# Performance work log

Hardware: AMD Instinct MI355X
Metric: run time of the kernel (lower is better)

The kernel has to match this reference:

```python
import jax, jax.numpy as jnp
import numpy as np

B, D, C = 32768, 1024, 40  # batch, proj_dim, num_classes('culture')


def setup_inputs() -> dict:
    key = jax.random.key(0)
    k1, k2, k3, k4, k5 = jax.random.split(key, 5)
    scale = 1.0 / np.sqrt(D)
    return {
        "src": jax.random.normal(k1, (B, D), dtype=jnp.float32),
        "attn_mask": jnp.ones((B,), dtype=jnp.float32),  # unpacked but unused by BiChain
        # padded weights: row i uses only first D+i columns; the rest hit zero buffer slots
        "W": jax.random.normal(k2, (C, D + C), dtype=jnp.float32) * scale,
        "b": jax.random.normal(k3, (C,), dtype=jnp.float32) * scale,
        "W_rev": jax.random.normal(k4, (C, D + C), dtype=jnp.float32) * scale,
        "b_rev": jax.random.normal(k5, (C,), dtype=jnp.float32) * scale,
    }


def _chain(src, W, b):
    """Sequential classifier chain: score_i = sigmoid(<[src, s_0..s_{i-1}], w_i> + b_i)."""
    Bsz, Df = src.shape
    Cn = W.shape[0]
    # growing feature buffer, pre-padded with zeros for future scores
    buf0 = jnp.zeros((Bsz, Df + Cn), dtype=src.dtype).at[:, :Df].set(src)

    def step(buf, inp):
        w_i, b_i, i = inp
        score = jax.nn.sigmoid(buf @ w_i + b_i)            # [B]
        buf = jax.lax.dynamic_update_slice(buf, score[:, None], (0, Df + i))
        return buf, score

    _, scores = jax.lax.scan(step, buf0, (W, b, jnp.arange(Cn)))
    return scores.T  # [B, C]


def reference(src, attn_mask, W, b, W_rev, b_rev):
    out_fwd = _chain(src, W, b)
    out_rev = _chain(src, W_rev, b_rev)
    return (out_fwd + out_rev[:, ::-1]) * 0.5
```

## Files before the change

kernel.cpp:

```cpp
#include <hip/hip_runtime.h>
#include <hip/hip_bf16.h>
#include <math.h>

using short8  = __attribute__((ext_vector_type(8))) short;
using float4v = __attribute__((ext_vector_type(4))) float;

#define D_DIM 1024
#define NCLS  40
#define WSTR  1064
#define TM    64
#define NCHUNK 16

typedef const __attribute__((address_space(1))) void g_void;
typedef __attribute__((address_space(3))) void lds_void;

__device__ __forceinline__ short f2bf(float f) {
    __hip_bfloat16 h = __float2bfloat16(f);
    union { __hip_bfloat16 h; short s; } u; u.h = h;
    return u.s;
}

__global__ void convert_w_kernel(const float* __restrict__ W, const float* __restrict__ Wr,
                                 short* __restrict__ Wfrag) {
    int idx  = blockIdx.x * 256 + threadIdx.x;
    int lane = idx & 63;
    int rest = idx >> 6;
    int t    = rest % 5;
    int rest2 = rest / 5;
    int ks   = rest2 & 1;
    int ch   = rest2 >> 1;
    int cls  = t * 16 + (lane & 15);
    int k0   = ch * 64 + ks * 32 + (lane >> 4) * 8;
    const float* srow = (cls < NCLS) ? (W + (size_t)cls * WSTR)
                                     : (Wr + (size_t)(cls - NCLS) * WSTR);
    short8 v;
#pragma unroll
    for (int e = 0; e < 8; ++e) v[e] = f2bf(srow[k0 + e]);
    *(short8*)(Wfrag + (size_t)idx * 8) = v;
}

__global__ __launch_bounds__(256, 2) void bichain_main(
    const float* __restrict__ src, const short* __restrict__ Wfrag,
    const float* __restrict__ Wf, const float* __restrict__ Wr,
    const float* __restrict__ bf_, const float* __restrict__ br_,
    float* __restrict__ out)
{
    __shared__ __align__(16) char smem[32768];

    const int tid  = threadIdx.x;
    const int lane = tid & 63;
    const int wave = tid >> 6;
    const int row0 = blockIdx.x * TM;
    const int lrow = lane & 15;
    const int g4   = lane >> 4;

    float4v acc[5];
#pragma unroll
    for (int t = 0; t < 5; ++t)
#pragma unroll
        for (int r = 0; r < 4; ++r) acc[t][r] = 0.f;

    auto stage = [&](int ch, int buf) {
        char* dst0 = smem + buf * 16384 + wave * 4096;
#pragma unroll
        for (int j = 0; j < 4; ++j) {
            int r   = wave * 16 + j * 4 + g4;
            int j16 = lrow ^ (r & 7);
            const float* gp = src + (size_t)(row0 + r) * D_DIM + ch * 64 + j16 * 4;
            __builtin_amdgcn_global_load_lds((g_void*)gp, (lds_void*)(dst0 + j * 1024),
                                             16, 0, 0);
        }
    };

    stage(0, 0);
    __syncthreads();

#pragma unroll 2
    for (int ch = 0; ch < NCHUNK; ++ch) {
        const int buf = ch & 1;
        short8 wfr[2][5];
#pragma unroll
        for (int ks = 0; ks < 2; ++ks)
#pragma unroll
            for (int t = 0; t < 5; ++t)
                wfr[ks][t] = *(const short8*)(Wfrag +
                                (((size_t)(ch * 2 + ks) * 5 + t) << 9) + (lane << 3));
        if (ch < NCHUNK - 1) stage(ch + 1, buf ^ 1);

        const char* Ab = smem + buf * 16384 + (wave * 16 + lrow) * 256;
#pragma unroll
        for (int ks = 0; ks < 2; ++ks) {
            float4v f0 = *(const float4v*)(Ab + (((ks * 8 + g4 * 2 + 0) ^ (lrow & 7)) << 4));
            float4v f1 = *(const float4v*)(Ab + (((ks * 8 + g4 * 2 + 1) ^ (lrow & 7)) << 4));
            short8 af;
#pragma unroll
            for (int e = 0; e < 4; ++e) { af[e] = f2bf(f0[e]); af[e + 4] = f2bf(f1[e]); }
#pragma unroll
            for (int t = 0; t < 5; ++t)
                acc[t] = __builtin_amdgcn_mfma_f32_16x16x32_bf16(af, wfr[ks][t], acc[t], 0, 0, 0);
        }
        __syncthreads();
    }

    float* Lg = (float*)smem;
#pragma unroll
    for (int t = 0; t < 5; ++t)
#pragma unroll
        for (int r = 0; r < 4; ++r) {
            int row = wave * 16 + g4 * 4 + r;
            int cls = t * 16 + lrow;
            Lg[row * 81 + cls] = acc[t][r];
        }
    __syncthreads();

    if (tid < 128) {
        const int row = tid >> 1;
        const int dir = tid & 1;
        const float* Wt = dir ? Wr : Wf;
        const float* bi = dir ? br_ : bf_;
        float s[NCLS];
#pragma unroll
        for (int i = 0; i < NCLS; ++i) {
            float z = Lg[row * 81 + dir * NCLS + i] + bi[i];
#pragma unroll
            for (int j = 0; j < i; ++j)
                z += s[j] * Wt[i * WSTR + D_DIM + j];
            s[i] = 1.f / (1.f + __expf(-z));
            Lg[row * 81 + dir * NCLS + i] = s[i];
        }
    }
    __syncthreads();

    float* outp = out + (size_t)row0 * NCLS;
    for (int idx = tid; idx < TM * NCLS; idx += 256) {
        int row = idx / NCLS;
        int c   = idx - row * NCLS;
        outp[idx] = 0.5f * (Lg[row * 81 + c] + Lg[row * 81 + NCLS + (NCLS - 1 - c)]);
    }
}

extern "C" void kernel_launch(void* const* d_in, const int* in_sizes, int n_in,
                              void* d_out, int out_size, void* d_ws, size_t ws_size,
                              hipStream_t stream) {
    const float* src = (const float*)d_in[0];
    const float* W   = (const float*)d_in[2];
    const float* b   = (const float*)d_in[3];
    const float* Wr  = (const float*)d_in[4];
    const float* br  = (const float*)d_in[5];
    float* out = (float*)d_out;
    short* Wfrag = (short*)d_ws;

    convert_w_kernel<<<40, 256, 0, stream>>>(W, Wr, Wfrag);
    bichain_main<<<512, 256, 0, stream>>>(src, Wfrag, W, Wr, b, br, out);
}
```

Before: 45.31 us.

## Replace LDS DMA staging with register-prefetched, wave-private bf16 LDS ring

The block-wide double-buffered global_load_lds staging of fp32 activations is replaced by register prefetch three chunks ahead. Each wave converts its rows to bf16 and writes them into its own private three-slot LDS ring, with the weight fragments double-buffered in registers. Because each wave only reads its own LDS slice, the per-chunk __syncthreads is removed, and the loop is fully unrolled to keep more global loads in flight. The cost is much higher register pressure from the prefetch arrays, which could lower occupancy below the launch-bounds target or cause spills.

```diff
diff --git a/kernel.cpp b/kernel.cpp
--- a/kernel.cpp
+++ b/kernel.cpp
@@ -2,17 +2,15 @@
 #include <hip/hip_bf16.h>
 #include <math.h>
 
-using short8  = __attribute__((ext_vector_type(8))) short;
-using float4v = __attribute__((ext_vector_type(4))) float;
+using short8   = __attribute__((ext_vector_type(8))) short;
+using ushort4v = __attribute__((ext_vector_type(4))) unsigned short;
+using float4v  = __attribute__((ext_vector_type(4))) float;
 
 #define D_DIM 1024
 #define NCLS  40
 #define WSTR  1064
 #define TM    64
-#define NCHUNK 16
-
-typedef const __attribute__((address_space(1))) void g_void;
-typedef __attribute__((address_space(3))) void lds_void;
+#define NCH   16
 
 __device__ __forceinline__ short f2bf(float f) {
     __hip_bfloat16 h = __float2bfloat16(f);
@@ -45,70 +43,99 @@
     const float* __restrict__ bf_, const float* __restrict__ br_,
     float* __restrict__ out)
 {
-    __shared__ __align__(16) char smem[32768];
+    __shared__ __align__(16) char smem[24576];
 
     const int tid  = threadIdx.x;
     const int lane = tid & 63;
     const int wave = tid >> 6;
     const int row0 = blockIdx.x * TM;
-    const int lrow = lane & 15;
-    const int g4   = lane >> 4;
+    const int i16  = lane & 15;
+    const int i4   = lane >> 4;
 
+    char* ldsW = smem + wave * 6144;
+    const float* aGlob = src + (size_t)(row0 + wave * 16 + i4) * D_DIM + i16 * 4;
+
+    float4v ap[3][4];
+    short8  wp[2][10];
     float4v acc[5];
 #pragma unroll
     for (int t = 0; t < 5; ++t)
 #pragma unroll
         for (int r = 0; r < 4; ++r) acc[t][r] = 0.f;
 
-    auto stage = [&](int ch, int buf) {
-        char* dst0 = smem + buf * 16384 + wave * 4096;
-#pragma unroll
-        for (int j = 0; j < 4; ++j) {
-            int r   = wave * 16 + j * 4 + g4;
-            int j16 = lrow ^ (r & 7);
-            const float* gp = src + (size_t)(row0 + r) * D_DIM + ch * 64 + j16 * 4;
-            __builtin_amdgcn_global_load_lds((g_void*)gp, (lds_void*)(dst0 + j * 1024),
-                                             16, 0, 0);
-        }
-    };
+#define LOADA(ch) do { if ((ch) < NCH) {                                   \
+    const float* _p = aGlob + (ch) * 64;                                   \
+    ap[(ch)%3][0] = *(const float4v*)(_p);                                 \
+    ap[(ch)%3][1] = *(const float4v*)(_p + 4 * D_DIM);                     \
+    ap[(ch)%3][2] = *(const float4v*)(_p + 8 * D_DIM);                     \
+    ap[(ch)%3][3] = *(const float4v*)(_p + 12 * D_DIM); } } while (0)
 
-    stage(0, 0);
+#define LOADW(ch) do { if ((ch) < NCH) {                                   \
+    const short* _w = Wfrag + (size_t)(ch) * 5120 + (lane << 3);           \
+    wp[(ch)%2][0] = *(const short8*)(_w + 0 * 512);                        \
+    wp[(ch)%2][1] = *(const short8*)(_w + 1 * 512);                        \
+    wp[(ch)%2][2] = *(const short8*)(_w + 2 * 512);                        \
+    wp[(ch)%2][3] = *(const short8*)(_w + 3 * 512);                        \
+    wp[(ch)%2][4] = *(const short8*)(_w + 4 * 512);                        \
+    wp[(ch)%2][5] = *(const short8*)(_w + 5 * 512);                        \
+    wp[(ch)%2][6] = *(const short8*)(_w + 6 * 512);                        \
+    wp[(ch)%2][7] = *(const short8*)(_w + 7 * 512);                        \
+    wp[(ch)%2][8] = *(const short8*)(_w + 8 * 512);                        \
+    wp[(ch)%2][9] = *(const short8*)(_w + 9 * 512); } } while (0)
+
+#define DSW1(ch, j) {                                                      \
+    int _r = (j) * 4 + i4;                                                 \
+    ushort4v _v;                                                           \
+    _v[0] = (unsigned short)f2bf(ap[(ch)%3][j][0]);                        \
+    _v[1] = (unsigned short)f2bf(ap[(ch)%3][j][1]);                        \
+    _v[2] = (unsigned short)f2bf(ap[(ch)%3][j][2]);                        \
+    _v[3] = (unsigned short)f2bf(ap[(ch)%3][j][3]);                        \
+    *(ushort4v*)(_b + _r * 128 + ((i16 ^ ((_r & 7) << 1)) << 3)) = _v; }
+#define DSW(ch) do { if ((ch) < NCH) {                                     \
+    char* _b = ldsW + ((ch)%3) * 2048;                                     \
+    DSW1(ch, 0) DSW1(ch, 1) DSW1(ch, 2) DSW1(ch, 3) } } while (0)
+
+#define MFMA_(ch) do {                                                     \
+    const char* _fb = ldsW + ((ch)%3) * 2048 + i16 * 128;                  \
+    const int _sw = (i16 & 7) << 1;                                        \
+    short8 _a0 = *(const short8*)(_fb + (((i4 * 2)     ^ _sw) << 3));      \
+    acc[0] = __builtin_amdgcn_mfma_f32_16x16x32_bf16(_a0, wp[(ch)%2][0], acc[0], 0, 0, 0); \
+    acc[1] = __builtin_amdgcn_mfma_f32_16x16x32_bf16(_a0, wp[(ch)%2][1], acc[1], 0, 0, 0); \
+    acc[2] = __builtin_amdgcn_mfma_f32_16x16x32_bf16(_a0, wp[(ch)%2][2], acc[2], 0, 0, 0); \
+    acc[3] = __builtin_amdgcn_mfma_f32_16x16x32_bf16(_a0, wp[(ch)%2][3], acc[3], 0, 0, 0); \
+    acc[4] = __builtin_amdgcn_mfma_f32_16x16x32_bf16(_a0, wp[(ch)%2][4], acc[4], 0, 0, 0); \
+    short8 _a1 = *(const short8*)(_fb + (((8 + i4 * 2) ^ _sw) << 3));      \
+    acc[0] = __builtin_amdgcn_mfma_f32_16x16x32_bf16(_a1, wp[(ch)%2][5], acc[0], 0, 0, 0); \
+    acc[1] = __builtin_amdgcn_mfma_f32_16x16x32_bf16(_a1, wp[(ch)%2][6], acc[1], 0, 0, 0); \
+    acc[2] = __builtin_amdgcn_mfma_f32_16x16x32_bf16(_a1, wp[(ch)%2][7], acc[2], 0, 0, 0); \
+    acc[3] = __builtin_amdgcn_mfma_f32_16x16x32_bf16(_a1, wp[(ch)%2][8], acc[3], 0, 0, 0); \
+    acc[4] = __builtin_amdgcn_mfma_f32_16x16x32_bf16(_a1, wp[(ch)%2][9], acc[4], 0, 0, 0); \
+  } while (0)
+
+#define BODY(ch) do { LOADW((ch)+1); LOADA((ch)+3); DSW((ch)+1); MFMA_(ch); } while (0)
+
+    LOADA(0); LOADA(1); LOADA(2); LOADW(0); DSW(0);
+    BODY(0);  BODY(1);  BODY(2);  BODY(3);
+    BODY(4);  BODY(5);  BODY(6);  BODY(7);
+    BODY(8);  BODY(9);  BODY(10); BODY(11);
+    BODY(12); BODY(13); BODY(14); BODY(15);
+
+#undef LOADA
+#undef LOADW
+#undef DSW1
+#undef DSW
+#undef MFMA_
+#undef BODY
+
     __syncthreads();
-
-#pragma unroll 2
-    for (int ch = 0; ch < NCHUNK; ++ch) {
-        const int buf = ch & 1;
-        short8 wfr[2][5];
-#pragma unroll
-        for (int ks = 0; ks < 2; ++ks)
-#pragma unroll
-            for (int t = 0; t < 5; ++t)
-                wfr[ks][t] = *(const short8*)(Wfrag +
-                                (((size_t)(ch * 2 + ks) * 5 + t) << 9) + (lane << 3));
-        if (ch < NCHUNK - 1) stage(ch + 1, buf ^ 1);
-
-        const char* Ab = smem + buf * 16384 + (wave * 16 + lrow) * 256;
-#pragma unroll
-        for (int ks = 0; ks < 2; ++ks) {
-            float4v f0 = *(const float4v*)(Ab + (((ks * 8 + g4 * 2 + 0) ^ (lrow & 7)) << 4));
-            float4v f1 = *(const float4v*)(Ab + (((ks * 8 + g4 * 2 + 1) ^ (lrow & 7)) << 4));
-            short8 af;
-#pragma unroll
-            for (int e = 0; e < 4; ++e) { af[e] = f2bf(f0[e]); af[e + 4] = f2bf(f1[e]); }
-#pragma unroll
-            for (int t = 0; t < 5; ++t)
-                acc[t] = __builtin_amdgcn_mfma_f32_16x16x32_bf16(af, wfr[ks][t], acc[t], 0, 0, 0);
-        }
-        __syncthreads();
-    }
 
     float* Lg = (float*)smem;
 #pragma unroll
     for (int t = 0; t < 5; ++t)
 #pragma unroll
         for (int r = 0; r < 4; ++r) {
-            int row = wave * 16 + g4 * 4 + r;
-            int cls = t * 16 + lrow;
+            int row = wave * 16 + i4 * 4 + r;
+            int cls = t * 16 + i16;
             Lg[row * 81 + cls] = acc[t][r];
         }
     __syncthreads();
```

After: 43.33 us. 1.05x faster.

## Split K across waves with 16-row tiles and register-prefetched bf16 LDS staging

Applied to the files above, without the earlier changes.

Reworks the main GEMM so each block handles 16 rows and the four waves split the 1024-wide reduction dimension, with partial accumulators reduced through LDS afterwards. The source tile is now loaded into registers, converted to bf16 before being written to a swizzled LDS buffer, and prefetched by a fully unrolled software pipeline in place of global_load_lds double buffering. Grid grows to 2048 blocks and occupancy hint rises to 4. The trade-off is an extra cross-wave reduction and a much shorter sequential chain phase per block (32 active threads), in exchange for more blocks, better latency hiding and half-size LDS traffic for A.

```diff
diff --git a/kernel.cpp b/kernel.cpp
--- a/kernel.cpp
+++ b/kernel.cpp
@@ -2,17 +2,15 @@
 #include <hip/hip_bf16.h>
 #include <math.h>
 
-using short8  = __attribute__((ext_vector_type(8))) short;
-using float4v = __attribute__((ext_vector_type(4))) float;
+using short8   = __attribute__((ext_vector_type(8))) short;
+using ushort4v = __attribute__((ext_vector_type(4))) unsigned short;
+using float4v  = __attribute__((ext_vector_type(4))) float;
 
 #define D_DIM 1024
 #define NCLS  40
 #define WSTR  1064
-#define TM    64
-#define NCHUNK 16
-
-typedef const __attribute__((address_space(1))) void g_void;
-typedef __attribute__((address_space(3))) void lds_void;
+#define TM    16
+#define BATCH 32768
 
 __device__ __forceinline__ short f2bf(float f) {
     __hip_bfloat16 h = __float2bfloat16(f);
@@ -26,11 +24,9 @@
     int lane = idx & 63;
     int rest = idx >> 6;
     int t    = rest % 5;
-    int rest2 = rest / 5;
-    int ks   = rest2 & 1;
-    int ch   = rest2 >> 1;
+    int kk   = rest / 5;
     int cls  = t * 16 + (lane & 15);
-    int k0   = ch * 64 + ks * 32 + (lane >> 4) * 8;
+    int k0   = kk * 32 + (lane >> 4) * 8;
     const float* srow = (cls < NCLS) ? (W + (size_t)cls * WSTR)
                                      : (Wr + (size_t)(cls - NCLS) * WSTR);
     short8 v;
@@ -39,81 +35,113 @@
     *(short8*)(Wfrag + (size_t)idx * 8) = v;
 }
 
-__global__ __launch_bounds__(256, 2) void bichain_main(
+__global__ __launch_bounds__(256, 4) void bichain_fused(
     const float* __restrict__ src, const short* __restrict__ Wfrag,
     const float* __restrict__ Wf, const float* __restrict__ Wr,
     const float* __restrict__ bf_, const float* __restrict__ br_,
     float* __restrict__ out)
 {
-    __shared__ __align__(16) char smem[32768];
+    __shared__ __align__(16) char smem[25664];
 
     const int tid  = threadIdx.x;
     const int lane = tid & 63;
     const int wave = tid >> 6;
     const int row0 = blockIdx.x * TM;
-    const int lrow = lane & 15;
-    const int g4   = lane >> 4;
+    const int i16  = lane & 15;
+    const int i4   = lane >> 4;
+    const int kw   = wave * 256;
 
+    char* ldsA = smem + wave * 4096;
+    const float* aGlob = src + (size_t)(row0 + i4) * D_DIM + kw + i16 * 4;
+
+    float4v ap[2][4];
+    short8  wp[2][5];
     float4v acc[5];
 #pragma unroll
     for (int t = 0; t < 5; ++t)
 #pragma unroll
         for (int r = 0; r < 4; ++r) acc[t][r] = 0.f;
 
-    auto stage = [&](int ch, int buf) {
-        char* dst0 = smem + buf * 16384 + wave * 4096;
-#pragma unroll
-        for (int j = 0; j < 4; ++j) {
-            int r   = wave * 16 + j * 4 + g4;
-            int j16 = lrow ^ (r & 7);
-            const float* gp = src + (size_t)(row0 + r) * D_DIM + ch * 64 + j16 * 4;
-            __builtin_amdgcn_global_load_lds((g_void*)gp, (lds_void*)(dst0 + j * 1024),
-                                             16, 0, 0);
-        }
-    };
+#define LOADA(c) do { if ((c) < 4) {                                       \
+    const float* _p = aGlob + (c) * 64;                                    \
+    ap[(c)&1][0] = *(const float4v*)(_p);                                  \
+    ap[(c)&1][1] = *(const float4v*)(_p + 4 * D_DIM);                      \
+    ap[(c)&1][2] = *(const float4v*)(_p + 8 * D_DIM);                      \
+    ap[(c)&1][3] = *(const float4v*)(_p + 12 * D_DIM); } } while (0)
 
-    stage(0, 0);
+#define LOADW(b) do { if ((b) < 8) {                                       \
+    const short* _w = Wfrag + ((size_t)(wave * 8 + (b)) * 5 * 512) + (lane << 3); \
+    wp[(b)&1][0] = *(const short8*)(_w + 0 * 512);                         \
+    wp[(b)&1][1] = *(const short8*)(_w + 1 * 512);                         \
+    wp[(b)&1][2] = *(const short8*)(_w + 2 * 512);                         \
+    wp[(b)&1][3] = *(const short8*)(_w + 3 * 512);                         \
+    wp[(b)&1][4] = *(const short8*)(_w + 4 * 512); } } while (0)
+
+#define DSW1(c, j) {                                                       \
+    int _r = (j) * 4 + i4;                                                 \
+    ushort4v _v;                                                           \
+    _v[0] = (unsigned short)f2bf(ap[(c)&1][j][0]);                         \
+    _v[1] = (unsigned short)f2bf(ap[(c)&1][j][1]);                         \
+    _v[2] = (unsigned short)f2bf(ap[(c)&1][j][2]);                         \
+    _v[3] = (unsigned short)f2bf(ap[(c)&1][j][3]);                         \
+    *(ushort4v*)(_b + _r * 128 + ((i16 ^ ((_r & 7) << 1)) << 3)) = _v; }
+#define DSW(c) do { if ((c) < 4) {                                         \
+    char* _b = ldsA + ((c)&1) * 2048;                                      \
+    DSW1(c, 0) DSW1(c, 1) DSW1(c, 2) DSW1(c, 3) } } while (0)
+
+#define MFMA_(b) do {                                                      \
+    const char* _fb = ldsA + (((b) >> 1) & 1) * 2048 + i16 * 128;          \
+    const int _sw = (i16 & 7) << 1;                                        \
+    short8 _a = *(const short8*)(_fb + (((((b)&1) * 8 + i4 * 2)) ^ _sw) * 8); \
+    acc[0] = __builtin_amdgcn_mfma_f32_16x16x32_bf16(_a, wp[(b)&1][0], acc[0], 0, 0, 0); \
+    acc[1] = __builtin_amdgcn_mfma_f32_16x16x32_bf16(_a, wp[(b)&1][1], acc[1], 0, 0, 0); \
+    acc[2] = __builtin_amdgcn_mfma_f32_16x16x32_bf16(_a, wp[(b)&1][2], acc[2], 0, 0, 0); \
+    acc[3] = __builtin_amdgcn_mfma_f32_16x16x32_bf16(_a, wp[(b)&1][3], acc[3], 0, 0, 0); \
+    acc[4] = __builtin_amdgcn_mfma_f32_16x16x32_bf16(_a, wp[(b)&1][4], acc[4], 0, 0, 0); \
+  } while (0)
+
+    LOADA(0); LOADA(1); LOADW(0); DSW(0);
+    LOADW(1); LOADA(2); MFMA_(0);
+    LOADW(2); DSW(1);   MFMA_(1);
+    LOADW(3); LOADA(3); MFMA_(2);
+    LOADW(4); DSW(2);   MFMA_(3);
+    LOADW(5);           MFMA_(4);
+    LOADW(6); DSW(3);   MFMA_(5);
+    LOADW(7);           MFMA_(6);
+                        MFMA_(7);
+
+#undef LOADA
+#undef LOADW
+#undef DSW1
+#undef DSW
+#undef MFMA_
+
     __syncthreads();
 
-#pragma unroll 2
-    for (int ch = 0; ch < NCHUNK; ++ch) {
-        const int buf = ch & 1;
-        short8 wfr[2][5];
-#pragma unroll
-        for (int ks = 0; ks < 2; ++ks)
-#pragma unroll
-            for (int t = 0; t < 5; ++t)
-                wfr[ks][t] = *(const short8*)(Wfrag +
-                                (((size_t)(ch * 2 + ks) * 5 + t) << 9) + (lane << 3));
-        if (ch < NCHUNK - 1) stage(ch + 1, buf ^ 1);
-
-        const char* Ab = smem + buf * 16384 + (wave * 16 + lrow) * 256;
-#pragma unroll
-        for (int ks = 0; ks < 2; ++ks) {
-            float4v f0 = *(const float4v*)(Ab + (((ks * 8 + g4 * 2 + 0) ^ (lrow & 7)) << 4));
-            float4v f1 = *(const float4v*)(Ab + (((ks * 8 + g4 * 2 + 1) ^ (lrow & 7)) << 4));
-            short8 af;
-#pragma unroll
-            for (int e = 0; e < 4; ++e) { af[e] = f2bf(f0[e]); af[e + 4] = f2bf(f1[e]); }
-#pragma unroll
-            for (int t = 0; t < 5; ++t)
-                acc[t] = __builtin_amdgcn_mfma_f32_16x16x32_bf16(af, wfr[ks][t], acc[t], 0, 0, 0);
-        }
-        __syncthreads();
-    }
-
-    float* Lg = (float*)smem;
+    float4v* Red = (float4v*)smem;
 #pragma unroll
     for (int t = 0; t < 5; ++t)
-#pragma unroll
-        for (int r = 0; r < 4; ++r) {
-            int row = wave * 16 + g4 * 4 + r;
-            int cls = t * 16 + lrow;
-            Lg[row * 81 + cls] = acc[t][r];
-        }
+        Red[(wave * 5 + t) * 64 + lane] = acc[t];
     __syncthreads();
 
-    if (tid < 128) {
+    float* Lg = (float*)(smem + 20480);
+    for (int item = tid; item < 320; item += 256) {
+        int t = item >> 6, l = item & 63;
+        float4v v = Red[t * 64 + l];
+#pragma unroll
+        for (int w = 1; w < 4; ++w) {
+            float4v u = Red[(w * 5 + t) * 64 + l];
+#pragma unroll
+            for (int r = 0; r < 4; ++r) v[r] += u[r];
+        }
+        int cls = t * 16 + (l & 15);
+        int rw  = (l >> 4) * 4;
+#pragma unroll
+        for (int r = 0; r < 4; ++r) Lg[(rw + r) * 81 + cls] = v[r];
+    }
+    __syncthreads();
+
+    if (tid < 32) {
         const int row = tid >> 1;
         const int dir = tid & 1;
         const float* Wt = dir ? Wr : Wf;
@@ -133,8 +161,7 @@
 
     float* outp = out + (size_t)row0 * NCLS;
     for (int idx = tid; idx < TM * NCLS; idx += 256) {
-        int row = idx / NCLS;
-        int c   = idx - row * NCLS;
+        int row = idx / NCLS, c = idx - row * NCLS;
         outp[idx] = 0.5f * (Lg[row * 81 + c] + Lg[row * 81 + NCLS + (NCLS - 1 - c)]);
     }
 }
@@ -151,5 +178,5 @@
     short* Wfrag = (short*)d_ws;
 
     convert_w_kernel<<<40, 256, 0, stream>>>(W, Wr, Wfrag);
-    bichain_main<<<512, 256, 0, stream>>>(src, Wfrag, W, Wr, b, br, out);
+    bichain_fused<<<BATCH / TM, 256, 0, stream>>>(src, Wfrag, W, Wr, b, br, out);
 }
```

Measured after the change: 62.23 us. 1.37x slower.

## Register-prefetch src chunks, convert to bf16 once into per-wave LDS, drop block syncs

Applied to the files above, without the earlier changes.

The main loop is restructured. Each wave now loads its own 16 rows of src into registers in 256-column chunks, converts them to bf16 once, and writes them into a per-wave swizzled LDS double buffer. This replaces the block-wide async global-to-LDS staging and the per-iteration __syncthreads. Weight fragments are prefetched one k-step ahead, and the fully unrolled schedule uses sched_barriers so the next chunk's global loads overlap the current MFMAs. The cost is many more registers (16 float4 plus weights), which may lower occupancy, and it relies on same-wave LDS ordering without a barrier.

```diff
diff --git a/kernel.cpp b/kernel.cpp
--- a/kernel.cpp
+++ b/kernel.cpp
@@ -2,17 +2,15 @@
 #include <hip/hip_bf16.h>
 #include <math.h>
 
-using short8  = __attribute__((ext_vector_type(8))) short;
-using float4v = __attribute__((ext_vector_type(4))) float;
+using short8   = __attribute__((ext_vector_type(8))) short;
+using ushort4v = __attribute__((ext_vector_type(4))) unsigned short;
+using float4v  = __attribute__((ext_vector_type(4))) float;
 
 #define D_DIM 1024
 #define NCLS  40
 #define WSTR  1064
 #define TM    64
-#define NCHUNK 16
-
-typedef const __attribute__((address_space(1))) void g_void;
-typedef __attribute__((address_space(3))) void lds_void;
+#define CW    256
 
 __device__ __forceinline__ short f2bf(float f) {
     __hip_bfloat16 h = __float2bfloat16(f);
@@ -26,11 +24,9 @@
     int lane = idx & 63;
     int rest = idx >> 6;
     int t    = rest % 5;
-    int rest2 = rest / 5;
-    int ks   = rest2 & 1;
-    int ch   = rest2 >> 1;
+    int kk   = rest / 5;
     int cls  = t * 16 + (lane & 15);
-    int k0   = ch * 64 + ks * 32 + (lane >> 4) * 8;
+    int k0   = kk * 32 + (lane >> 4) * 8;
     const float* srow = (cls < NCLS) ? (W + (size_t)cls * WSTR)
                                      : (Wr + (size_t)(cls - NCLS) * WSTR);
     short8 v;
@@ -45,70 +41,91 @@
     const float* __restrict__ bf_, const float* __restrict__ br_,
     float* __restrict__ out)
 {
-    __shared__ __align__(16) char smem[32768];
+    __shared__ __align__(16) char smem[65536];
 
     const int tid  = threadIdx.x;
     const int lane = tid & 63;
     const int wave = tid >> 6;
     const int row0 = blockIdx.x * TM;
-    const int lrow = lane & 15;
-    const int g4   = lane >> 4;
+    const int i16  = lane & 15;
+    const int i4   = lane >> 4;
+    const int sw7  = i16 & 7;
 
+    char* ldsW = smem + wave * 16384;
+    const float* aBase = src + (size_t)(row0 + wave * 16) * D_DIM + lane * 4;
+
+    float4v ap[16];
+    short8  wp[2][5];
     float4v acc[5];
 #pragma unroll
     for (int t = 0; t < 5; ++t)
 #pragma unroll
         for (int r = 0; r < 4; ++r) acc[t][r] = 0.f;
 
-    auto stage = [&](int ch, int buf) {
-        char* dst0 = smem + buf * 16384 + wave * 4096;
+    auto loadA = [&](int ch) {
+        const float* p = aBase + ch * CW;
 #pragma unroll
-        for (int j = 0; j < 4; ++j) {
-            int r   = wave * 16 + j * 4 + g4;
-            int j16 = lrow ^ (r & 7);
-            const float* gp = src + (size_t)(row0 + r) * D_DIM + ch * 64 + j16 * 4;
-            __builtin_amdgcn_global_load_lds((g_void*)gp, (lds_void*)(dst0 + j * 1024),
-                                             16, 0, 0);
+        for (int r = 0; r < 16; ++r)
+            ap[r] = *(const float4v*)(p + (size_t)r * D_DIM);
+    };
+    auto dsw = [&](int bufi) {
+        char* b = ldsW + bufi * 8192;
+        const int so = (lane >> 1);
+#pragma unroll
+        for (int r = 0; r < 16; ++r) {
+            ushort4v v;
+            v[0] = (unsigned short)f2bf(ap[r][0]);
+            v[1] = (unsigned short)f2bf(ap[r][1]);
+            v[2] = (unsigned short)f2bf(ap[r][2]);
+            v[3] = (unsigned short)f2bf(ap[r][3]);
+            *(ushort4v*)(b + r * 512 + ((so ^ (r & 7)) << 4) + (lane & 1) * 8) = v;
         }
     };
 
-    stage(0, 0);
+#define LOADW(kk, sl) do { if ((kk) < 32) {                                \
+    const short* _w = Wfrag + (size_t)(kk) * 2560 + (lane << 3);           \
+    wp[sl][0] = *(const short8*)(_w + 0 * 512);                            \
+    wp[sl][1] = *(const short8*)(_w + 1 * 512);                            \
+    wp[sl][2] = *(const short8*)(_w + 2 * 512);                            \
+    wp[sl][3] = *(const short8*)(_w + 3 * 512);                            \
+    wp[sl][4] = *(const short8*)(_w + 4 * 512); } } while (0)
+
+#define MFMAK(ch, ks) do {                                                 \
+    const char* _fb = ldsW + ((ch) & 1) * 8192 + i16 * 512;                \
+    short8 _a = *(const short8*)(_fb + ((((ks) * 4 + i4) ^ sw7) << 4));    \
+    acc[0] = __builtin_amdgcn_mfma_f32_16x16x32_bf16(_a, wp[(ks)&1][0], acc[0], 0, 0, 0); \
+    acc[1] = __builtin_amdgcn_mfma_f32_16x16x32_bf16(_a, wp[(ks)&1][1], acc[1], 0, 0, 0); \
+    acc[2] = __builtin_amdgcn_mfma_f32_16x16x32_bf16(_a, wp[(ks)&1][2], acc[2], 0, 0, 0); \
+    acc[3] = __builtin_amdgcn_mfma_f32_16x16x32_bf16(_a, wp[(ks)&1][3], acc[3], 0, 0, 0); \
+    acc[4] = __builtin_amdgcn_mfma_f32_16x16x32_bf16(_a, wp[(ks)&1][4], acc[4], 0, 0, 0); \
+  } while (0)
+
+#define CSTEP(ch, ks) do { LOADW((ch) * 8 + (ks) + 1, ((ks) + 1) & 1); MFMAK(ch, ks); } while (0)
+#define COMPUTE(ch) do { CSTEP(ch,0); CSTEP(ch,1); CSTEP(ch,2); CSTEP(ch,3);               \
+                         CSTEP(ch,4); CSTEP(ch,5); CSTEP(ch,6); CSTEP(ch,7); } while (0)
+#define SB __builtin_amdgcn_sched_barrier(0)
+
+    loadA(0); dsw(0); LOADW(0, 0);
+    loadA(1); SB; COMPUTE(0); dsw(1);
+    loadA(2); SB; COMPUTE(1); dsw(0);
+    loadA(3); SB; COMPUTE(2); dsw(1);
+               SB; COMPUTE(3);
+
+#undef LOADW
+#undef MFMAK
+#undef CSTEP
+#undef COMPUTE
+#undef SB
+
     __syncthreads();
-
-#pragma unroll 2
-    for (int ch = 0; ch < NCHUNK; ++ch) {
-        const int buf = ch & 1;
-        short8 wfr[2][5];
-#pragma unroll
-        for (int ks = 0; ks < 2; ++ks)
-#pragma unroll
-            for (int t = 0; t < 5; ++t)
-                wfr[ks][t] = *(const short8*)(Wfrag +
-                                (((size_t)(ch * 2 + ks) * 5 + t) << 9) + (lane << 3));
-        if (ch < NCHUNK - 1) stage(ch + 1, buf ^ 1);
-
-        const char* Ab = smem + buf * 16384 + (wave * 16 + lrow) * 256;
-#pragma unroll
-        for (int ks = 0; ks < 2; ++ks) {
-            float4v f0 = *(const float4v*)(Ab + (((ks * 8 + g4 * 2 + 0) ^ (lrow & 7)) << 4));
-            float4v f1 = *(const float4v*)(Ab + (((ks * 8 + g4 * 2 + 1) ^ (lrow & 7)) << 4));
-            short8 af;
-#pragma unroll
-            for (int e = 0; e < 4; ++e) { af[e] = f2bf(f0[e]); af[e + 4] = f2bf(f1[e]); }
-#pragma unroll
-            for (int t = 0; t < 5; ++t)
-                acc[t] = __builtin_amdgcn_mfma_f32_16x16x32_bf16(af, wfr[ks][t], acc[t], 0, 0, 0);
-        }
-        __syncthreads();
-    }
 
     float* Lg = (float*)smem;
 #pragma unroll
     for (int t = 0; t < 5; ++t)
 #pragma unroll
         for (int r = 0; r < 4; ++r) {
-            int row = wave * 16 + g4 * 4 + r;
-            int cls = t * 16 + lrow;
+            int row = wave * 16 + i4 * 4 + r;
+            int cls = t * 16 + i16;
             Lg[row * 81 + cls] = acc[t][r];
         }
     __syncthreads();
```

Measured after the change: 47.42 us. 1.05x slower.
